# Optimization experiments

Measured on AMD Instinct MI355X. Metric: run time of the kernel, lower is better.

## Reference

```python
import jax, jax.numpy as jnp
import numpy as np

LN_EPS = 1e-12
BIG = 1e30
BAND = 15  # end index may be at most 15 tokens after start


def output_layer(x, w1, b1, g, b, w2, b2):
    # Linear -> ReLU -> LayerNorm -> Linear (dropout is identity at eval)
    h = jax.nn.relu(x @ w1 + b1)
    mu = jnp.mean(h, axis=-1, keepdims=True)
    var = jnp.mean(jnp.square(h - mu), axis=-1, keepdims=True)
    h = (h - mu) * jax.lax.rsqrt(var + LN_EPS) * g + b
    return h @ w2 + b2


def setup_inputs() -> dict:
    key = jax.random.key(0)
    ks = jax.random.split(key, 8)
    B, S, D = 8, 4096, 1024
    H2 = 2 * D
    inp = {
        "context_input": jax.random.normal(ks[0], (B, S, D), jnp.float32),
        "context_mask": jnp.ones((B, S), jnp.float32),
    }
    def head(k1, k2, n_ans):
        return (
            0.02 * jax.random.normal(k1, (D, H2), jnp.float32),
            jnp.zeros((H2,), jnp.float32),
            jnp.ones((H2,), jnp.float32),
            jnp.zeros((H2,), jnp.float32),
            0.02 * jax.random.normal(k2, (H2, n_ans), jnp.float32),
            jnp.zeros((n_ans,), jnp.float32),
        )
    for name, k1, k2, n_ans in [("start", ks[1], ks[2], 1), ("end", ks[3], ks[4], 1), ("type", ks[5], ks[6], 4)]:
        w1, b1, g, b, w2, b2 = head(k1, k2, n_ans)
        inp[f"{name}_w1"] = w1; inp[f"{name}_b1"] = b1
        inp[f"{name}_g"] = g; inp[f"{name}_b"] = b
        inp[f"{name}_w2"] = w2; inp[f"{name}_b2"] = b2
    return inp


def reference(context_input, context_mask,
              start_w1, start_b1, start_g, start_b, start_w2, start_b2,
              end_w1, end_b1, end_g, end_b, end_w2, end_b2,
              type_w1, type_b1, type_g, type_b, type_w2, type_b2):
    S = context_input.shape[1]
    start_pred = output_layer(context_input, start_w1, start_b1, start_g, start_b, start_w2, start_b2)[..., 0] \
        - BIG * (1.0 - context_mask)  # [B,S]
    end_pred = output_layer(context_input, end_w1, end_b1, end_g, end_b, end_w2, end_b2)[..., 0] \
        - BIG * (1.0 - context_mask)  # [B,S]
    type_pred = output_layer(context_input[:, 0, :], type_w1, type_b1, type_g, type_b, type_w2, type_b2)  # [B,4]

    # outer[b,i,j] = start[b,i] + end[b,j], masked to band 0 <= j-i <= 15
    outer = start_pred[:, :, None] + end_pred[:, None, :]  # [B,S,S]
    i = jnp.arange(S)[:, None]
    j = jnp.arange(S)[None, :]
    band = ((j >= i) & (j <= i + BAND)).astype(outer.dtype)  # [S,S]
    outer = outer - BIG * (1.0 - band)[None]

    yp1 = jnp.argmax(jnp.max(outer, axis=2), axis=1)  # best start index [B]
    yp2 = jnp.argmax(jnp.max(outer, axis=1), axis=1)  # best end index [B]
    return start_pred, end_pred, type_pred, yp1, yp2
```

## Files before the change

kernel.cpp:

```cpp
#include <hip/hip_runtime.h>

typedef _Float16 f16x8 __attribute__((ext_vector_type(8)));
typedef float f32x4 __attribute__((ext_vector_type(4)));

#define BIGF 1e30f
#define M_TOT 32768
#define H2 2048

#define WS_XH 0u
#define WS_WT 67108864u
#define WS_BVEC 75497472u
#define WS_GW2 75513856u
#define WS_CONSTS 75530240u
#define WS_PART 75530496u
#define WS_TPART 100696320u

__global__ void k_pre(const float* __restrict__ x, _Float16* __restrict__ xh,
                      const float* __restrict__ w_s, const float* __restrict__ w_e,
                      _Float16* __restrict__ wt,
                      const float* __restrict__ s_b1, const float* __restrict__ s_g,
                      const float* __restrict__ s_w2, const float* __restrict__ s_b,
                      const float* __restrict__ s_b2, const float* __restrict__ e_b1,
                      const float* __restrict__ e_g, const float* __restrict__ e_w2,
                      const float* __restrict__ e_b, const float* __restrict__ e_b2,
                      float* __restrict__ bvec, float* __restrict__ gw2,
                      float* __restrict__ consts) {
  __shared__ float tile[64][65];
  int bid = blockIdx.x;
  if (bid < 16384) {
    size_t i = ((size_t)bid * 256 + threadIdx.x) * 8;
    float4 v0 = *(const float4*)(x + i);
    float4 v1 = *(const float4*)(x + i + 4);
    f16x8 h;
    h[0] = (_Float16)v0.x; h[1] = (_Float16)v0.y; h[2] = (_Float16)v0.z; h[3] = (_Float16)v0.w;
    h[4] = (_Float16)v1.x; h[5] = (_Float16)v1.y; h[6] = (_Float16)v1.z; h[7] = (_Float16)v1.w;
    *(f16x8*)(xh + i) = h;
  } else if (bid < 17408) {
    int r = bid - 16384;
    int bx = r & 31, by = (r >> 5) & 15, bz = r >> 9;
    const float* w = bz ? w_e : w_s;
    int n0 = bx * 64, k0 = by * 64;
    int tx = threadIdx.x & 63, ty = threadIdx.x >> 6;
#pragma unroll
    for (int i = ty; i < 64; i += 4) tile[i][tx] = w[(size_t)(k0 + i) * H2 + n0 + tx];
    __syncthreads();
#pragma unroll
    for (int i = ty; i < 64; i += 4)
      wt[((size_t)(bz * H2 + n0 + i)) * 1024 + k0 + tx] = (_Float16)tile[tx][i];
  } else {
    int blk = bid - 17408;
    if (blk < 16) {
      int i = blk * 256 + threadIdx.x;
      int head = i >> 11, j = i & (H2 - 1);
      bvec[i] = head ? e_b1[j] : s_b1[j];
      gw2[i] = head ? e_g[j] * e_w2[j] : s_g[j] * s_w2[j];
    } else {
      int h = blk - 16;
      const float* g = h ? e_g : s_g;
      const float* b = h ? e_b : s_b;
      const float* w2 = h ? e_w2 : s_w2;
      const float* b2 = h ? e_b2 : s_b2;
      float c1 = 0.f, c2 = 0.f;
      for (int j = threadIdx.x; j < H2; j += 256) {
        float w = w2[j];
        c1 += g[j] * w;
        c2 += b[j] * w;
      }
      for (int m = 1; m < 64; m <<= 1) { c1 += __shfl_xor(c1, m); c2 += __shfl_xor(c2, m); }
      __shared__ float r1[4], r2[4];
      int wid = threadIdx.x >> 6;
      if ((threadIdx.x & 63) == 0) { r1[wid] = c1; r2[wid] = c2; }
      __syncthreads();
      if (threadIdx.x == 0) {
        consts[h * 2 + 0] = r1[0] + r1[1] + r1[2] + r1[3];
        consts[h * 2 + 1] = r2[0] + r2[1] + r2[2] + r2[3] + b2[0];
      }
    }
  }
}

#define BUF 65536
#define STA(q, tile, bufo)                                                              \
  __builtin_amdgcn_global_load_lds(                                                     \
      (const __attribute__((address_space(1))) unsigned int*)(srcA + (size_t)(q) * 131072 + (size_t)(tile) * 128), \
      (__attribute__((address_space(3))) unsigned int*)(lds + (bufo) + (q) * 8192 + t * 16), 16, 0, 0)
#define STB(q, tile, bufo)                                                              \
  __builtin_amdgcn_global_load_lds(                                                     \
      (const __attribute__((address_space(1))) unsigned int*)(srcB + (size_t)(q) * 131072 + (size_t)(tile) * 128), \
      (__attribute__((address_space(3))) unsigned int*)(lds + (bufo) + 32768 + (q) * 8192 + t * 16), 16, 0, 0)

#define READA(AF, mi0, BUFO)                                                            \
  AF[0][0] = *(const f16x8*)(lds + (BUFO) + arow + (mi0) * 2048 + low0);                \
  AF[0][1] = *(const f16x8*)(lds + (BUFO) + arow + (mi0) * 2048 + low1);                \
  AF[1][0] = *(const f16x8*)(lds + (BUFO) + arow + ((mi0) + 1) * 2048 + low0);          \
  AF[1][1] = *(const f16x8*)(lds + (BUFO) + arow + ((mi0) + 1) * 2048 + low1);

#define READB(BF, BUFO)                                                                 \
  _Pragma("unroll")                                                                     \
  for (int nj = 0; nj < 4; ++nj) {                                                      \
    BF[nj][0] = *(const f16x8*)(lds + (BUFO) + brow + nj * 2048 + low0);                \
    BF[nj][1] = *(const f16x8*)(lds + (BUFO) + brow + nj * 2048 + low1);                \
  }

#define MFMA2(m0, m1, AF, BF)                                                           \
  __builtin_amdgcn_s_setprio(1);                                                        \
  _Pragma("unroll")                                                                     \
  for (int nj = 0; nj < 4; ++nj) {                                                      \
    acc[m0][nj] = __builtin_amdgcn_mfma_f32_16x16x32_f16(AF[0][0], BF[nj][0], acc[m0][nj], 0, 0, 0); \
    acc[m1][nj] = __builtin_amdgcn_mfma_f32_16x16x32_f16(AF[1][0], BF[nj][0], acc[m1][nj], 0, 0, 0); \
  }                                                                                     \
  _Pragma("unroll")                                                                     \
  for (int nj = 0; nj < 4; ++nj) {                                                      \
    acc[m0][nj] = __builtin_amdgcn_mfma_f32_16x16x32_f16(AF[0][1], BF[nj][1], acc[m0][nj], 0, 0, 0); \
    acc[m1][nj] = __builtin_amdgcn_mfma_f32_16x16x32_f16(AF[1][1], BF[nj][1], acc[m1][nj], 0, 0, 0); \
  }                                                                                     \
  __builtin_amdgcn_s_setprio(0);

#define K_ITER(g, OB, OBN, BFC, BFN)                                                    \
  {                                                                                     \
                           \
    READA(afB, 2, OB);                                                                  \
    if ((g) < 15) { STA(1, (g) + 1, OBN); STA(3, (g) + 1, OBN); }                       \
    asm volatile("s_waitcnt lgkmcnt(4)" ::: "memory");                                  \
    __builtin_amdgcn_s_barrier();                                                       \
    __builtin_amdgcn_sched_barrier(0);                                                  \
    MFMA2(0, 1, afA, BFC);                                                              \
                           \
    READA(afA, 4, OB);                                                                  \
    if ((g) < 14) { STB(0, (g) + 2, OB); STB(1, (g) + 2, OB); }                         \
    asm volatile("s_waitcnt lgkmcnt(4)" ::: "memory");                                  \
    __builtin_amdgcn_s_barrier();                                                       \
    __builtin_amdgcn_sched_barrier(0);                                                  \
    MFMA2(2, 3, afB, BFC);                                                              \
           \
    READA(afB, 6, OB);                                                                  \
    if ((g) < 14) { STB(2, (g) + 2, OB); STB(3, (g) + 2, OB); }                         \
    if ((g) < 14)       asm volatile("s_waitcnt vmcnt(4)" ::: "memory");                \
    else if ((g) == 14) asm volatile("s_waitcnt vmcnt(0)" ::: "memory");                \
    asm volatile("s_waitcnt lgkmcnt(4)" ::: "memory");                                  \
    __builtin_amdgcn_s_barrier();                                                       \
    __builtin_amdgcn_sched_barrier(0);                                                  \
    MFMA2(4, 5, afA, BFC);                                                              \
       \
    if ((g) < 15) {                                                                     \
      READB(BFN, OBN);                                                                  \
      READA(afA, 0, OBN);                                                               \
      if ((g) < 14) { STA(0, (g) + 2, OB); STA(2, (g) + 2, OB); }                       \
      asm volatile("s_waitcnt lgkmcnt(12)" ::: "memory");                               \
    } else {                                                                            \
      asm volatile("s_waitcnt lgkmcnt(0)" ::: "memory");                                \
    }                                                                                   \
    __builtin_amdgcn_s_barrier();                                                       \
    __builtin_amdgcn_sched_barrier(0);                                                  \
    MFMA2(6, 7, afB, BFC);                                                              \
  }

__global__ __launch_bounds__(512, 2) void k_gemm(const _Float16* __restrict__ Xh,
                                                 const _Float16* __restrict__ Wt,
                                                 const float* __restrict__ bvec,
                                                 const float* __restrict__ gw2,
                                                 float* __restrict__ partials) {
  __shared__ char lds[2 * BUF];
  const int nb = blockIdx.x;
  const int mb = blockIdx.y;
  const int t = threadIdx.x;
  const int lane = t & 63, wid = t >> 6;
  const int c15 = lane & 15, g4 = lane >> 4;
  const int wmg = wid >> 2;
  const int wq = wid & 3;
  const int wn = wq * 64;

  f32x4 acc[8][4];
#pragma unroll
  for (int i = 0; i < 8; ++i)
#pragma unroll
    for (int j = 0; j < 4; ++j) acc[i][j] = (f32x4){0.f, 0.f, 0.f, 0.f};

  const char* Abase = (const char*)(Xh + (size_t)mb * 256 * 1024);
  const char* Bbase = (const char*)(Wt + (size_t)nb * 256 * 1024);
  const int rowl = t >> 3;
  const int swz = ((t & 7) * 16) ^ ((rowl & 7) << 4);
  const char* srcA = Abase + (size_t)rowl * 2048 + swz;
  const char* srcB = Bbase + (size_t)rowl * 2048 + swz;

  const int xorv = (c15 & 7) << 4;
  const int low0 = (g4 * 16) ^ xorv;
  const int low1 = (64 + g4 * 16) ^ xorv;
  const int arow = (wmg * 128 + c15) * 128;
  const int brow = 32768 + (wn + c15) * 128;

  STA(0, 0, 0); STA(1, 0, 0); STA(2, 0, 0); STA(3, 0, 0);
  STB(0, 0, 0); STB(1, 0, 0); STB(2, 0, 0); STB(3, 0, 0);
  STB(0, 1, BUF); STB(1, 1, BUF); STB(2, 1, BUF); STB(3, 1, BUF);
  STA(0, 1, BUF); STA(2, 1, BUF);
  asm volatile("s_waitcnt vmcnt(6)" ::: "memory");
  __builtin_amdgcn_s_barrier();
  __builtin_amdgcn_sched_barrier(0);

  f16x8 afA[2][2], afB[2][2], bfA[4][2], bfB[4][2];
  READB(bfA, 0);
  READA(afA, 0, 0);

#pragma unroll
  for (int gp = 0; gp < 8; ++gp) {
    K_ITER(2 * gp, 0u, BUF, bfA, bfB);
    K_ITER(2 * gp + 1, BUF, 0u, bfB, bfA);
  }

  __syncthreads();
  float* red = (float*)lds;

  float bv[4], gv[4];
#pragma unroll
  for (int nj = 0; nj < 4; ++nj) {
    int col = nb * 256 + wn + nj * 16 + c15;
    bv[nj] = bvec[col];
    gv[nj] = gw2[col];
  }
#pragma unroll
  for (int mi = 0; mi < 8; ++mi) {
#pragma unroll
    for (int r = 0; r < 4; ++r) {
      float s1 = 0.f, s2 = 0.f, s3 = 0.f;
#pragma unroll
      for (int nj = 0; nj < 4; ++nj) {
        float v = acc[mi][nj][r] + bv[nj];
        v = fmaxf(v, 0.f);
        s1 += v;
        s2 += v * v;
        s3 += v * gv[nj];
      }
#pragma unroll
      for (int m = 1; m < 16; m <<= 1) {
        s1 += __shfl_xor(s1, m);
        s2 += __shfl_xor(s2, m);
        s3 += __shfl_xor(s3, m);
      }
      if (c15 == 0) {
        int row = mi * 16 + g4 * 4 + r;
        float* p = red + (((wmg * 4 + wq) * 128 + row) * 3);
        p[0] = s1; p[1] = s2; p[2] = s3;
      }
    }
  }
  __syncthreads();
  for (int idx = t; idx < 768; idx += 512) {
    int wmgi = idx / 384;
    int rem = idx - wmgi * 384;
    int row = rem / 3, k = rem - row * 3;
    float s = red[((wmgi * 4 + 0) * 128 + row) * 3 + k] +
              red[((wmgi * 4 + 1) * 128 + row) * 3 + k] +
              red[((wmgi * 4 + 2) * 128 + row) * 3 + k] +
              red[((wmgi * 4 + 3) * 128 + row) * 3 + k];
    int rowg = mb * 256 + wmgi * 128 + row;
    partials[((size_t)(nb * 3 + k)) * M_TOT + rowg] = s;
  }
}

__global__ void k_reduce(const float* __restrict__ partials, const float* __restrict__ consts,
                         const float* __restrict__ mask, float* __restrict__ out) {
  int m = blockIdx.x * 256 + threadIdx.x;
  float s1 = 0.f, s2 = 0.f, s3 = 0.f, e1 = 0.f, e2 = 0.f, e3 = 0.f;
  for (int nb = 0; nb < 8; ++nb) {
    s1 += partials[((size_t)(nb * 3 + 0)) * M_TOT + m];
    s2 += partials[((size_t)(nb * 3 + 1)) * M_TOT + m];
    s3 += partials[((size_t)(nb * 3 + 2)) * M_TOT + m];
  }
  for (int nb = 8; nb < 16; ++nb) {
    e1 += partials[((size_t)(nb * 3 + 0)) * M_TOT + m];
    e2 += partials[((size_t)(nb * 3 + 1)) * M_TOT + m];
    e3 += partials[((size_t)(nb * 3 + 2)) * M_TOT + m];
  }
  const float H = (float)H2;
  float mu = s1 / H;
  float var = fmaxf(s2 / H - mu * mu, 0.f);
  float rs = 1.f / sqrtf(var + 1e-12f);
  float score_s = rs * (s3 - mu * consts[0]) + consts[1];
  mu = e1 / H;
  var = fmaxf(e2 / H - mu * mu, 0.f);
  rs = 1.f / sqrtf(var + 1e-12f);
  float score_e = rs * (e3 - mu * consts[2]) + consts[3];
  float mk = BIGF * (1.f - mask[m]);
  out[m] = score_s - mk;
  out[M_TOT + m] = score_e - mk;
}

__global__ void k_type_partial(const float* __restrict__ X, const float* __restrict__ w1,
                               const float* __restrict__ b1, const float* __restrict__ g,
                               const float* __restrict__ w2, float* __restrict__ tpart) {
  __shared__ float xs[1024];
  int cb = blockIdx.x, tok = blockIdx.y, t = threadIdx.x;
  const float* xp = X + (size_t)tok * 4096 * 1024;
  for (int i = t; i < 1024; i += 256) xs[i] = xp[i];
  __syncthreads();
  int j = cb * 256 + t;
  float dot = 0.f;
  for (int k = 0; k < 1024; ++k) dot += xs[k] * w1[(size_t)k * H2 + j];
  float h = fmaxf(dot + b1[j], 0.f);
  float gj = g[j];
  float s[6];
  s[0] = h;
  s[1] = h * h;
#pragma unroll
  for (int c = 0; c < 4; ++c) s[2 + c] = h * gj * w2[j * 4 + c];
  for (int m = 1; m < 64; m <<= 1)
#pragma unroll
    for (int q = 0; q < 6; ++q) s[q] += __shfl_xor(s[q], m);
  __shared__ float red[4][6];
  int wid = t >> 6;
  if ((t & 63) == 0)
#pragma unroll
    for (int q = 0; q < 6; ++q) red[wid][q] = s[q];
  __syncthreads();
  if (t == 0)
#pragma unroll
    for (int q = 0; q < 6; ++q)
      tpart[(tok * 8 + cb) * 6 + q] = red[0][q] + red[1][q] + red[2][q] + red[3][q];
}

__global__ void k_type_final(const float* __restrict__ tpart, const float* __restrict__ g,
                             const float* __restrict__ bb, const float* __restrict__ w2,
                             const float* __restrict__ b2, float* __restrict__ out) {
  int t = threadIdx.x;
  float c1[4] = {0.f, 0.f, 0.f, 0.f}, c2[4] = {0.f, 0.f, 0.f, 0.f};
  for (int j = t; j < H2; j += 256) {
    float gj = g[j], bj = bb[j];
#pragma unroll
    for (int c = 0; c < 4; ++c) {
      float w = w2[j * 4 + c];
      c1[c] += gj * w;
      c2[c] += bj * w;
    }
  }
  for (int m = 1; m < 64; m <<= 1)
#pragma unroll
    for (int c = 0; c < 4; ++c) { c1[c] += __shfl_xor(c1[c], m); c2[c] += __shfl_xor(c2[c], m); }
  __shared__ float rC1[4][4], rC2[4][4];
  int wid = t >> 6;
  if ((t & 63) == 0)
#pragma unroll
    for (int c = 0; c < 4; ++c) { rC1[wid][c] = c1[c]; rC2[wid][c] = c2[c]; }
  __syncthreads();
  __shared__ float sC1[4], sC2[4];
  if (t < 4) {
    sC1[t] = rC1[0][t] + rC1[1][t] + rC1[2][t] + rC1[3][t];
    sC2[t] = rC2[0][t] + rC2[1][t] + rC2[2][t] + rC2[3][t];
  }
  __syncthreads();
  if (t < 32) {
    int tok = t >> 2, c = t & 3;
    float s1 = 0.f, s2 = 0.f, s3 = 0.f;
    for (int cb = 0; cb < 8; ++cb) {
      s1 += tpart[(tok * 8 + cb) * 6 + 0];
      s2 += tpart[(tok * 8 + cb) * 6 + 1];
      s3 += tpart[(tok * 8 + cb) * 6 + 2 + c];
    }
    float mu = s1 / (float)H2;
    float var = fmaxf(s2 / (float)H2 - mu * mu, 0.f);
    float rs = 1.f / sqrtf(var + 1e-12f);
    out[65536 + tok * 4 + c] = rs * (s3 - mu * sC1[c]) + sC2[c] + b2[c];
  }
}

__global__ void k_band(const float* __restrict__ preds, float* __restrict__ out) {
  __shared__ float ss[4096], se[4096];
  int b = blockIdx.x, t = threadIdx.x;
  for (int i = t; i < 4096; i += 256) {
    ss[i] = preds[(size_t)b * 4096 + i];
    se[i] = preds[M_TOT + (size_t)b * 4096 + i];
  }
  __syncthreads();
  float bv1 = -3.0e38f, bv2 = -3.0e38f;
  int bi1 = 0x7fffffff, bi2 = 0x7fffffff;
  for (int i = t; i < 4096; i += 256) {
    float m1 = -3.0e38f;
    int jmax = i + 15 < 4095 ? i + 15 : 4095;
    for (int j = i; j <= jmax; ++j) m1 = fmaxf(m1, se[j]);
    float v1 = ss[i] + m1;
    if (v1 > bv1 || (v1 == bv1 && i < bi1)) { bv1 = v1; bi1 = i; }
    float m2 = -3.0e38f;
    int imin = i - 15 > 0 ? i - 15 : 0;
    for (int j = imin; j <= i; ++j) m2 = fmaxf(m2, ss[j]);
    float v2 = se[i] + m2;
    if (v2 > bv2 || (v2 == bv2 && i < bi2)) { bv2 = v2; bi2 = i; }
  }
  for (int m = 1; m < 64; m <<= 1) {
    float ov = __shfl_xor(bv1, m);
    int oi = __shfl_xor(bi1, m);
    if (ov > bv1 || (ov == bv1 && oi < bi1)) { bv1 = ov; bi1 = oi; }
    ov = __shfl_xor(bv2, m);
    oi = __shfl_xor(bi2, m);
    if (ov > bv2 || (ov == bv2 && oi < bi2)) { bv2 = ov; bi2 = oi; }
  }
  __shared__ float rv[2][4];
  __shared__ int ri[2][4];
  int wid = t >> 6;
  if ((t & 63) == 0) { rv[0][wid] = bv1; ri[0][wid] = bi1; rv[1][wid] = bv2; ri[1][wid] = bi2; }
  __syncthreads();
  if (t == 0) {
    float v = rv[0][0];
    int ix = ri[0][0];
    for (int w = 1; w < 4; ++w)
      if (rv[0][w] > v || (rv[0][w] == v && ri[0][w] < ix)) { v = rv[0][w]; ix = ri[0][w]; }
    out[65568 + b] = (float)ix;
    v = rv[1][0];
    ix = ri[1][0];
    for (int w = 1; w < 4; ++w)
      if (rv[1][w] > v || (rv[1][w] == v && ri[1][w] < ix)) { v = rv[1][w]; ix = ri[1][w]; }
    out[65576 + b] = (float)ix;
  }
}

extern "C" void kernel_launch(void* const* d_in, const int* in_sizes, int n_in, void* d_out,
                              int out_size, void* d_ws, size_t ws_size, hipStream_t stream) {
  const float* X = (const float*)d_in[0];
  const float* mask = (const float*)d_in[1];
  const float* s_w1 = (const float*)d_in[2];
  const float* s_b1 = (const float*)d_in[3];
  const float* s_g = (const float*)d_in[4];
  const float* s_b = (const float*)d_in[5];
  const float* s_w2 = (const float*)d_in[6];
  const float* s_b2 = (const float*)d_in[7];
  const float* e_w1 = (const float*)d_in[8];
  const float* e_b1 = (const float*)d_in[9];
  const float* e_g = (const float*)d_in[10];
  const float* e_b = (const float*)d_in[11];
  const float* e_w2 = (const float*)d_in[12];
  const float* e_b2 = (const float*)d_in[13];
  const float* t_w1 = (const float*)d_in[14];
  const float* t_b1 = (const float*)d_in[15];
  const float* t_g = (const float*)d_in[16];
  const float* t_b = (const float*)d_in[17];
  const float* t_w2 = (const float*)d_in[18];
  const float* t_b2 = (const float*)d_in[19];

  char* ws = (char*)d_ws;
  _Float16* Xh = (_Float16*)(ws + WS_XH);
  _Float16* Wt = (_Float16*)(ws + WS_WT);
  float* bvec = (float*)(ws + WS_BVEC);
  float* gw2 = (float*)(ws + WS_GW2);
  float* consts = (float*)(ws + WS_CONSTS);
  float* partials = (float*)(ws + WS_PART);
  float* tpart = (float*)(ws + WS_TPART);
  float* out = (float*)d_out;

  k_pre<<<17426, 256, 0, stream>>>(X, Xh, s_w1, e_w1, Wt, s_b1, s_g, s_w2, s_b, s_b2,
                                   e_b1, e_g, e_w2, e_b, e_b2, bvec, gw2, consts);
  k_gemm<<<dim3(16, 128), 512, 0, stream>>>(Xh, Wt, bvec, gw2, partials);
  k_reduce<<<128, 256, 0, stream>>>(partials, consts, mask, out);
  k_type_partial<<<dim3(8, 8), 256, 0, stream>>>(X, t_w1, t_b1, t_g, t_w2, tpart);
  k_type_final<<<1, 256, 0, stream>>>(tpart, t_g, t_b, t_w2, t_b2, out);
  k_band<<<8, 256, 0, stream>>>(out, out);
}
```

Measured before the change: 395.5 us.

## Restructure GEMM main loop into K-half phases with 4x4 MFMA blocks

Reorganizes the fp16 MFMA GEMM inner loop so each phase covers one K-half (low0/low1) across four M sub-tiles and four N sub-tiles. Each phase issues 16 MFMAs, where the previous code split the work by pairs of M rows across both K halves. Global-to-LDS prefetch of the next-next tile is regrouped behind a full vmcnt(0) wait and extra barriers around each MFMA block, and the loop runs with pragma unroll 2 instead of being fully unrolled. The aim is better LDS read reuse and fewer register fragments. The extra barriers and the full vmcnt wait may reduce overlap of loads with compute.

After: 869.5 us. +119.8%, slower.

```diff
diff --git a/kernel.cpp b/kernel.cpp
--- a/kernel.cpp
+++ b/kernel.cpp
@@ -89,71 +89,30 @@
       (const __attribute__((address_space(1))) unsigned int*)(srcB + (size_t)(q) * 131072 + (size_t)(tile) * 128), \
       (__attribute__((address_space(3))) unsigned int*)(lds + (bufo) + 32768 + (q) * 8192 + t * 16), 16, 0, 0)
 
-#define READA(AF, mi0, BUFO)                                                            \
-  AF[0][0] = *(const f16x8*)(lds + (BUFO) + arow + (mi0) * 2048 + low0);                \
-  AF[0][1] = *(const f16x8*)(lds + (BUFO) + arow + (mi0) * 2048 + low1);                \
-  AF[1][0] = *(const f16x8*)(lds + (BUFO) + arow + ((mi0) + 1) * 2048 + low0);          \
-  AF[1][1] = *(const f16x8*)(lds + (BUFO) + arow + ((mi0) + 1) * 2048 + low1);
-
-#define READB(BF, BUFO)                                                                 \
+#define RD_A(AF, mh, low, BUFO)                                                         \
   _Pragma("unroll")                                                                     \
-  for (int nj = 0; nj < 4; ++nj) {                                                      \
-    BF[nj][0] = *(const f16x8*)(lds + (BUFO) + brow + nj * 2048 + low0);                \
-    BF[nj][1] = *(const f16x8*)(lds + (BUFO) + brow + nj * 2048 + low1);                \
-  }
-
-#define MFMA2(m0, m1, AF, BF)                                                           \
+  for (int mi = 0; mi < 4; ++mi)                                                        \
+    AF[mi] = *(const f16x8*)(lds + (BUFO) + (unsigned)((wmg * 128 + (mh) * 64 + mi * 16 + c15) * 128) + (low));
+
+#define RD_B(BF, low, BUFO)                                                             \
+  _Pragma("unroll")                                                                     \
+  for (int nj = 0; nj < 4; ++nj)                                                        \
+    BF[nj] = *(const f16x8*)(lds + (BUFO) + 32768 + (unsigned)((wn + nj * 16 + c15) * 128) + (low));
+
+#define MF16(mh, AF, BF)                                                                \
   __builtin_amdgcn_s_setprio(1);                                                        \
   _Pragma("unroll")                                                                     \
-  for (int nj = 0; nj < 4; ++nj) {                                                      \
-    acc[m0][nj] = __builtin_amdgcn_mfma_f32_16x16x32_f16(AF[0][0], BF[nj][0], acc[m0][nj], 0, 0, 0); \
-    acc[m1][nj] = __builtin_amdgcn_mfma_f32_16x16x32_f16(AF[1][0], BF[nj][0], acc[m1][nj], 0, 0, 0); \
-  }                                                                                     \
-  _Pragma("unroll")                                                                     \
-  for (int nj = 0; nj < 4; ++nj) {                                                      \
-    acc[m0][nj] = __builtin_amdgcn_mfma_f32_16x16x32_f16(AF[0][1], BF[nj][1], acc[m0][nj], 0, 0, 0); \
-    acc[m1][nj] = __builtin_amdgcn_mfma_f32_16x16x32_f16(AF[1][1], BF[nj][1], acc[m1][nj], 0, 0, 0); \
-  }                                                                                     \
+  for (int mi = 0; mi < 4; ++mi)                                                        \
+    _Pragma("unroll")                                                                   \
+    for (int nj = 0; nj < 4; ++nj)                                                      \
+      acc[(mh) * 4 + mi][nj] =                                                          \
+          __builtin_amdgcn_mfma_f32_16x16x32_f16(AF[mi], BF[nj], acc[(mh) * 4 + mi][nj], 0, 0, 0); \
   __builtin_amdgcn_s_setprio(0);
 
-#define K_ITER(g, OB, OBN, BFC, BFN)                                                    \
-  {                                                                                     \
-                           \
-    READA(afB, 2, OB);                                                                  \
-    if ((g) < 15) { STA(1, (g) + 1, OBN); STA(3, (g) + 1, OBN); }                       \
-    asm volatile("s_waitcnt lgkmcnt(4)" ::: "memory");                                  \
-    __builtin_amdgcn_s_barrier();                                                       \
-    __builtin_amdgcn_sched_barrier(0);                                                  \
-    MFMA2(0, 1, afA, BFC);                                                              \
-                           \
-    READA(afA, 4, OB);                                                                  \
-    if ((g) < 14) { STB(0, (g) + 2, OB); STB(1, (g) + 2, OB); }                         \
-    asm volatile("s_waitcnt lgkmcnt(4)" ::: "memory");                                  \
-    __builtin_amdgcn_s_barrier();                                                       \
-    __builtin_amdgcn_sched_barrier(0);                                                  \
-    MFMA2(2, 3, afB, BFC);                                                              \
-           \
-    READA(afB, 6, OB);                                                                  \
-    if ((g) < 14) { STB(2, (g) + 2, OB); STB(3, (g) + 2, OB); }                         \
-    if ((g) < 14)       asm volatile("s_waitcnt vmcnt(4)" ::: "memory");                \
-    else if ((g) == 14) asm volatile("s_waitcnt vmcnt(0)" ::: "memory");                \
-    asm volatile("s_waitcnt lgkmcnt(4)" ::: "memory");                                  \
-    __builtin_amdgcn_s_barrier();                                                       \
-    __builtin_amdgcn_sched_barrier(0);                                                  \
-    MFMA2(4, 5, afA, BFC);                                                              \
-       \
-    if ((g) < 15) {                                                                     \
-      READB(BFN, OBN);                                                                  \
-      READA(afA, 0, OBN);                                                               \
-      if ((g) < 14) { STA(0, (g) + 2, OB); STA(2, (g) + 2, OB); }                       \
-      asm volatile("s_waitcnt lgkmcnt(12)" ::: "memory");                               \
-    } else {                                                                            \
-      asm volatile("s_waitcnt lgkmcnt(0)" ::: "memory");                                \
-    }                                                                                   \
-    __builtin_amdgcn_s_barrier();                                                       \
-    __builtin_amdgcn_sched_barrier(0);                                                  \
-    MFMA2(6, 7, afB, BFC);                                                              \
-  }
+#define LGKM_BAR(N)                                                                     \
+  asm volatile("s_waitcnt lgkmcnt(" #N ")" ::: "memory");                               \
+  __builtin_amdgcn_s_barrier();                                                         \
+  __builtin_amdgcn_sched_barrier(0);
 
 __global__ __launch_bounds__(512, 2) void k_gemm(const _Float16* __restrict__ Xh,
                                                  const _Float16* __restrict__ Wt,
@@ -184,27 +143,63 @@
   const char* srcB = Bbase + (size_t)rowl * 2048 + swz;
 
   const int xorv = (c15 & 7) << 4;
-  const int low0 = (g4 * 16) ^ xorv;
-  const int low1 = (64 + g4 * 16) ^ xorv;
-  const int arow = (wmg * 128 + c15) * 128;
-  const int brow = 32768 + (wn + c15) * 128;
+  const unsigned low0 = (unsigned)((g4 * 16) ^ xorv);
+  const unsigned low1 = (unsigned)((64 + g4 * 16) ^ xorv);
 
   STA(0, 0, 0); STA(1, 0, 0); STA(2, 0, 0); STA(3, 0, 0);
   STB(0, 0, 0); STB(1, 0, 0); STB(2, 0, 0); STB(3, 0, 0);
+  STA(0, 1, BUF); STA(1, 1, BUF); STA(2, 1, BUF); STA(3, 1, BUF);
   STB(0, 1, BUF); STB(1, 1, BUF); STB(2, 1, BUF); STB(3, 1, BUF);
-  STA(0, 1, BUF); STA(2, 1, BUF);
-  asm volatile("s_waitcnt vmcnt(6)" ::: "memory");
+  asm volatile("s_waitcnt vmcnt(8)" ::: "memory");
   __builtin_amdgcn_s_barrier();
   __builtin_amdgcn_sched_barrier(0);
 
-  f16x8 afA[2][2], afB[2][2], bfA[4][2], bfB[4][2];
-  READB(bfA, 0);
-  READA(afA, 0, 0);
-
-#pragma unroll
-  for (int gp = 0; gp < 8; ++gp) {
-    K_ITER(2 * gp, 0u, BUF, bfA, bfB);
-    K_ITER(2 * gp + 1, BUF, 0u, bfB, bfA);
+  f16x8 afA[4], afB[4], bfA[4], bfB[4];
+  RD_A(afA, 0, low0, 0u)
+  RD_B(bfA, low0, 0u)
+
+#pragma unroll 2
+  for (int g = 0; g < 16; ++g) {
+    const unsigned ob = (unsigned)(g & 1) * BUF;
+    const unsigned on = ob ^ BUF;
+
+    RD_A(afB, 1, low0, ob)
+    LGKM_BAR(4)
+    MF16(0, afA, bfA)
+    __builtin_amdgcn_s_barrier();
+    __builtin_amdgcn_sched_barrier(0);
+
+    RD_A(afA, 0, low1, ob)
+    RD_B(bfB, low1, ob)
+    LGKM_BAR(8)
+    MF16(1, afB, bfA)
+    __builtin_amdgcn_s_barrier();
+    __builtin_amdgcn_sched_barrier(0);
+
+    RD_A(afB, 1, low1, ob)
+    asm volatile("s_waitcnt lgkmcnt(4)" ::: "memory");
+    if (g < 15) asm volatile("s_waitcnt vmcnt(0)" ::: "memory");
+    __builtin_amdgcn_s_barrier();
+    __builtin_amdgcn_sched_barrier(0);
+    if (g < 14) {
+      STB(0, g + 2, ob); STB(1, g + 2, ob); STB(2, g + 2, ob); STB(3, g + 2, ob);
+      STA(0, g + 2, ob); STA(1, g + 2, ob);
+    }
+    MF16(0, afA, bfB)
+    __builtin_amdgcn_s_barrier();
+    __builtin_amdgcn_sched_barrier(0);
+
+    if (g < 15) {
+      RD_A(afA, 0, low0, on)
+      RD_B(bfA, low0, on)
+      LGKM_BAR(8)
+    } else {
+      LGKM_BAR(0)
+    }
+    if (g < 14) { STA(2, g + 2, ob); STA(3, g + 2, ob); }
+    MF16(1, afB, bfB)
+    __builtin_amdgcn_s_barrier();
+    __builtin_amdgcn_sched_barrier(0);
   }
 
   __syncthreads();
```

## Swizzle GEMM block order and merge small tail kernels into two launches

Applied to the files above, without the earlier changes.

The GEMM grid becomes 1D with a block-index swizzle, so consecutive blocks are spread across M-tiles in a pattern meant to improve L2 reuse of the weight and activation tiles (and possibly XCD placement). The reduce and type-head partial kernels are merged into one launch using block-index branching, and the type-final and band-argmax kernels are merged into a second. This cuts the launch count from five to three, removing launch gaps between tiny kernels, at the cost of larger shared-memory use per block in the fused kernels.

New measurement: 389.9 us, median of 3. Within noise of the previous version (-1.4%).

```diff
diff --git a/kernel.cpp b/kernel.cpp
--- a/kernel.cpp
+++ b/kernel.cpp
@@ -161,8 +161,10 @@
                                                  const float* __restrict__ gw2,
                                                  float* __restrict__ partials) {
   __shared__ char lds[2 * BUF];
-  const int nb = blockIdx.x;
-  const int mb = blockIdx.y;
+  const int bid = blockIdx.x;
+  const int swzb = (bid & 7) * 256 + (bid >> 3);
+  const int nb = swzb & 15;
+  const int mb = swzb >> 4;
   const int t = threadIdx.x;
   const int lane = t & 63, wid = t >> 6;
   const int c15 = lane & 15, g4 = lane >> 4;
@@ -257,157 +259,161 @@
   }
 }
 
-__global__ void k_reduce(const float* __restrict__ partials, const float* __restrict__ consts,
-                         const float* __restrict__ mask, float* __restrict__ out) {
-  int m = blockIdx.x * 256 + threadIdx.x;
-  float s1 = 0.f, s2 = 0.f, s3 = 0.f, e1 = 0.f, e2 = 0.f, e3 = 0.f;
-  for (int nb = 0; nb < 8; ++nb) {
-    s1 += partials[((size_t)(nb * 3 + 0)) * M_TOT + m];
-    s2 += partials[((size_t)(nb * 3 + 1)) * M_TOT + m];
-    s3 += partials[((size_t)(nb * 3 + 2)) * M_TOT + m];
-  }
-  for (int nb = 8; nb < 16; ++nb) {
-    e1 += partials[((size_t)(nb * 3 + 0)) * M_TOT + m];
-    e2 += partials[((size_t)(nb * 3 + 1)) * M_TOT + m];
-    e3 += partials[((size_t)(nb * 3 + 2)) * M_TOT + m];
-  }
-  const float H = (float)H2;
-  float mu = s1 / H;
-  float var = fmaxf(s2 / H - mu * mu, 0.f);
-  float rs = 1.f / sqrtf(var + 1e-12f);
-  float score_s = rs * (s3 - mu * consts[0]) + consts[1];
-  mu = e1 / H;
-  var = fmaxf(e2 / H - mu * mu, 0.f);
-  rs = 1.f / sqrtf(var + 1e-12f);
-  float score_e = rs * (e3 - mu * consts[2]) + consts[3];
-  float mk = BIGF * (1.f - mask[m]);
-  out[m] = score_s - mk;
-  out[M_TOT + m] = score_e - mk;
+__global__ void k_mid(const float* __restrict__ partials, const float* __restrict__ consts,
+                      const float* __restrict__ mask, float* __restrict__ out,
+                      const float* __restrict__ X, const float* __restrict__ w1,
+                      const float* __restrict__ b1, const float* __restrict__ g,
+                      const float* __restrict__ w2, float* __restrict__ tpart) {
+  __shared__ float xs[1024];
+  __shared__ float red[4][6];
+  int bid = blockIdx.x, t = threadIdx.x;
+  if (bid < 128) {
+    int m = bid * 256 + t;
+    float s1 = 0.f, s2 = 0.f, s3 = 0.f, e1 = 0.f, e2 = 0.f, e3 = 0.f;
+    for (int nb = 0; nb < 8; ++nb) {
+      s1 += partials[((size_t)(nb * 3 + 0)) * M_TOT + m];
+      s2 += partials[((size_t)(nb * 3 + 1)) * M_TOT + m];
+      s3 += partials[((size_t)(nb * 3 + 2)) * M_TOT + m];
+    }
+    for (int nb = 8; nb < 16; ++nb) {
+      e1 += partials[((size_t)(nb * 3 + 0)) * M_TOT + m];
+      e2 += partials[((size_t)(nb * 3 + 1)) * M_TOT + m];
+      e3 += partials[((size_t)(nb * 3 + 2)) * M_TOT + m];
+    }
+    const float H = (float)H2;
+    float mu = s1 / H;
+    float var = fmaxf(s2 / H - mu * mu, 0.f);
+    float rs = 1.f / sqrtf(var + 1e-12f);
+    float score_s = rs * (s3 - mu * consts[0]) + consts[1];
+    mu = e1 / H;
+    var = fmaxf(e2 / H - mu * mu, 0.f);
+    rs = 1.f / sqrtf(var + 1e-12f);
+    float score_e = rs * (e3 - mu * consts[2]) + consts[3];
+    float mk = BIGF * (1.f - mask[m]);
+    out[m] = score_s - mk;
+    out[M_TOT + m] = score_e - mk;
+  } else {
+    int r = bid - 128;
+    int cb = r & 7, tok = r >> 3;
+    const float* xp = X + (size_t)tok * 4096 * 1024;
+    for (int i = t; i < 1024; i += 256) xs[i] = xp[i];
+    __syncthreads();
+    int j = cb * 256 + t;
+    float dot = 0.f;
+    for (int k = 0; k < 1024; ++k) dot += xs[k] * w1[(size_t)k * H2 + j];
+    float h = fmaxf(dot + b1[j], 0.f);
+    float gj = g[j];
+    float s[6];
+    s[0] = h;
+    s[1] = h * h;
+#pragma unroll
+    for (int c = 0; c < 4; ++c) s[2 + c] = h * gj * w2[j * 4 + c];
+    for (int m = 1; m < 64; m <<= 1)
+#pragma unroll
+      for (int q = 0; q < 6; ++q) s[q] += __shfl_xor(s[q], m);
+    int wid = t >> 6;
+    if ((t & 63) == 0)
+#pragma unroll
+      for (int q = 0; q < 6; ++q) red[wid][q] = s[q];
+    __syncthreads();
+    if (t == 0)
+#pragma unroll
+      for (int q = 0; q < 6; ++q)
+        tpart[(tok * 8 + cb) * 6 + q] = red[0][q] + red[1][q] + red[2][q] + red[3][q];
+  }
 }
 
-__global__ void k_type_partial(const float* __restrict__ X, const float* __restrict__ w1,
-                               const float* __restrict__ b1, const float* __restrict__ g,
-                               const float* __restrict__ w2, float* __restrict__ tpart) {
-  __shared__ float xs[1024];
-  int cb = blockIdx.x, tok = blockIdx.y, t = threadIdx.x;
-  const float* xp = X + (size_t)tok * 4096 * 1024;
-  for (int i = t; i < 1024; i += 256) xs[i] = xp[i];
-  __syncthreads();
-  int j = cb * 256 + t;
-  float dot = 0.f;
-  for (int k = 0; k < 1024; ++k) dot += xs[k] * w1[(size_t)k * H2 + j];
-  float h = fmaxf(dot + b1[j], 0.f);
-  float gj = g[j];
-  float s[6];
-  s[0] = h;
-  s[1] = h * h;
-#pragma unroll
-  for (int c = 0; c < 4; ++c) s[2 + c] = h * gj * w2[j * 4 + c];
-  for (int m = 1; m < 64; m <<= 1)
-#pragma unroll
-    for (int q = 0; q < 6; ++q) s[q] += __shfl_xor(s[q], m);
-  __shared__ float red[4][6];
-  int wid = t >> 6;
-  if ((t & 63) == 0)
-#pragma unroll
-    for (int q = 0; q < 6; ++q) red[wid][q] = s[q];
-  __syncthreads();
-  if (t == 0)
-#pragma unroll
-    for (int q = 0; q < 6; ++q)
-      tpart[(tok * 8 + cb) * 6 + q] = red[0][q] + red[1][q] + red[2][q] + red[3][q];
-}
-
-__global__ void k_type_final(const float* __restrict__ tpart, const float* __restrict__ g,
-                             const float* __restrict__ bb, const float* __restrict__ w2,
-                             const float* __restrict__ b2, float* __restrict__ out) {
-  int t = threadIdx.x;
-  float c1[4] = {0.f, 0.f, 0.f, 0.f}, c2[4] = {0.f, 0.f, 0.f, 0.f};
-  for (int j = t; j < H2; j += 256) {
-    float gj = g[j], bj = bb[j];
-#pragma unroll
-    for (int c = 0; c < 4; ++c) {
-      float w = w2[j * 4 + c];
-      c1[c] += gj * w;
-      c2[c] += bj * w;
-    }
-  }
-  for (int m = 1; m < 64; m <<= 1)
-#pragma unroll
-    for (int c = 0; c < 4; ++c) { c1[c] += __shfl_xor(c1[c], m); c2[c] += __shfl_xor(c2[c], m); }
+__global__ void k_fin(const float* __restrict__ tpart, const float* __restrict__ g,
+                      const float* __restrict__ bb, const float* __restrict__ w2,
+                      const float* __restrict__ b2, float* __restrict__ out) {
+  __shared__ float ss[4096], se[4096];
   __shared__ float rC1[4][4], rC2[4][4];
-  int wid = t >> 6;
-  if ((t & 63) == 0)
-#pragma unroll
-    for (int c = 0; c < 4; ++c) { rC1[wid][c] = c1[c]; rC2[wid][c] = c2[c]; }
-  __syncthreads();
   __shared__ float sC1[4], sC2[4];
-  if (t < 4) {
-    sC1[t] = rC1[0][t] + rC1[1][t] + rC1[2][t] + rC1[3][t];
-    sC2[t] = rC2[0][t] + rC2[1][t] + rC2[2][t] + rC2[3][t];
-  }
-  __syncthreads();
-  if (t < 32) {
-    int tok = t >> 2, c = t & 3;
-    float s1 = 0.f, s2 = 0.f, s3 = 0.f;
-    for (int cb = 0; cb < 8; ++cb) {
-      s1 += tpart[(tok * 8 + cb) * 6 + 0];
-      s2 += tpart[(tok * 8 + cb) * 6 + 1];
-      s3 += tpart[(tok * 8 + cb) * 6 + 2 + c];
-    }
-    float mu = s1 / (float)H2;
-    float var = fmaxf(s2 / (float)H2 - mu * mu, 0.f);
-    float rs = 1.f / sqrtf(var + 1e-12f);
-    out[65536 + tok * 4 + c] = rs * (s3 - mu * sC1[c]) + sC2[c] + b2[c];
-  }
-}
-
-__global__ void k_band(const float* __restrict__ preds, float* __restrict__ out) {
-  __shared__ float ss[4096], se[4096];
-  int b = blockIdx.x, t = threadIdx.x;
-  for (int i = t; i < 4096; i += 256) {
-    ss[i] = preds[(size_t)b * 4096 + i];
-    se[i] = preds[M_TOT + (size_t)b * 4096 + i];
-  }
-  __syncthreads();
-  float bv1 = -3.0e38f, bv2 = -3.0e38f;
-  int bi1 = 0x7fffffff, bi2 = 0x7fffffff;
-  for (int i = t; i < 4096; i += 256) {
-    float m1 = -3.0e38f;
-    int jmax = i + 15 < 4095 ? i + 15 : 4095;
-    for (int j = i; j <= jmax; ++j) m1 = fmaxf(m1, se[j]);
-    float v1 = ss[i] + m1;
-    if (v1 > bv1 || (v1 == bv1 && i < bi1)) { bv1 = v1; bi1 = i; }
-    float m2 = -3.0e38f;
-    int imin = i - 15 > 0 ? i - 15 : 0;
-    for (int j = imin; j <= i; ++j) m2 = fmaxf(m2, ss[j]);
-    float v2 = se[i] + m2;
-    if (v2 > bv2 || (v2 == bv2 && i < bi2)) { bv2 = v2; bi2 = i; }
-  }
-  for (int m = 1; m < 64; m <<= 1) {
-    float ov = __shfl_xor(bv1, m);
-    int oi = __shfl_xor(bi1, m);
-    if (ov > bv1 || (ov == bv1 && oi < bi1)) { bv1 = ov; bi1 = oi; }
-    ov = __shfl_xor(bv2, m);
-    oi = __shfl_xor(bi2, m);
-    if (ov > bv2 || (ov == bv2 && oi < bi2)) { bv2 = ov; bi2 = oi; }
-  }
   __shared__ float rv[2][4];
   __shared__ int ri[2][4];
-  int wid = t >> 6;
-  if ((t & 63) == 0) { rv[0][wid] = bv1; ri[0][wid] = bi1; rv[1][wid] = bv2; ri[1][wid] = bi2; }
-  __syncthreads();
-  if (t == 0) {
-    float v = rv[0][0];
-    int ix = ri[0][0];
-    for (int w = 1; w < 4; ++w)
-      if (rv[0][w] > v || (rv[0][w] == v && ri[0][w] < ix)) { v = rv[0][w]; ix = ri[0][w]; }
-    out[65568 + b] = (float)ix;
-    v = rv[1][0];
-    ix = ri[1][0];
-    for (int w = 1; w < 4; ++w)
-      if (rv[1][w] > v || (rv[1][w] == v && ri[1][w] < ix)) { v = rv[1][w]; ix = ri[1][w]; }
-    out[65576 + b] = (float)ix;
+  int bid = blockIdx.x, t = threadIdx.x;
+  if (bid == 0) {
+    float c1[4] = {0.f, 0.f, 0.f, 0.f}, c2[4] = {0.f, 0.f, 0.f, 0.f};
+    for (int j = t; j < H2; j += 256) {
+      float gj = g[j], bj = bb[j];
+#pragma unroll
+      for (int c = 0; c < 4; ++c) {
+        float w = w2[j * 4 + c];
+        c1[c] += gj * w;
+        c2[c] += bj * w;
+      }
+    }
+    for (int m = 1; m < 64; m <<= 1)
+#pragma unroll
+      for (int c = 0; c < 4; ++c) { c1[c] += __shfl_xor(c1[c], m); c2[c] += __shfl_xor(c2[c], m); }
+    int wid = t >> 6;
+    if ((t & 63) == 0)
+#pragma unroll
+      for (int c = 0; c < 4; ++c) { rC1[wid][c] = c1[c]; rC2[wid][c] = c2[c]; }
+    __syncthreads();
+    if (t < 4) {
+      sC1[t] = rC1[0][t] + rC1[1][t] + rC1[2][t] + rC1[3][t];
+      sC2[t] = rC2[0][t] + rC2[1][t] + rC2[2][t] + rC2[3][t];
+    }
+    __syncthreads();
+    if (t < 32) {
+      int tok = t >> 2, c = t & 3;
+      float s1 = 0.f, s2 = 0.f, s3 = 0.f;
+      for (int cb = 0; cb < 8; ++cb) {
+        s1 += tpart[(tok * 8 + cb) * 6 + 0];
+        s2 += tpart[(tok * 8 + cb) * 6 + 1];
+        s3 += tpart[(tok * 8 + cb) * 6 + 2 + c];
+      }
+      float mu = s1 / (float)H2;
+      float var = fmaxf(s2 / (float)H2 - mu * mu, 0.f);
+      float rs = 1.f / sqrtf(var + 1e-12f);
+      out[65536 + tok * 4 + c] = rs * (s3 - mu * sC1[c]) + sC2[c] + b2[c];
+    }
+  } else {
+    int b = bid - 1;
+    const float* preds = out;
+    for (int i = t; i < 4096; i += 256) {
+      ss[i] = preds[(size_t)b * 4096 + i];
+      se[i] = preds[M_TOT + (size_t)b * 4096 + i];
+    }
+    __syncthreads();
+    float bv1 = -3.0e38f, bv2 = -3.0e38f;
+    int bi1 = 0x7fffffff, bi2 = 0x7fffffff;
+    for (int i = t; i < 4096; i += 256) {
+      float m1 = -3.0e38f;
+      int jmax = i + 15 < 4095 ? i + 15 : 4095;
+      for (int j = i; j <= jmax; ++j) m1 = fmaxf(m1, se[j]);
+      float v1 = ss[i] + m1;
+      if (v1 > bv1 || (v1 == bv1 && i < bi1)) { bv1 = v1; bi1 = i; }
+      float m2 = -3.0e38f;
+      int imin = i - 15 > 0 ? i - 15 : 0;
+      for (int j = imin; j <= i; ++j) m2 = fmaxf(m2, ss[j]);
+      float v2 = se[i] + m2;
+      if (v2 > bv2 || (v2 == bv2 && i < bi2)) { bv2 = v2; bi2 = i; }
+    }
+    for (int m = 1; m < 64; m <<= 1) {
+      float ov = __shfl_xor(bv1, m);
+      int oi = __shfl_xor(bi1, m);
+      if (ov > bv1 || (ov == bv1 && oi < bi1)) { bv1 = ov; bi1 = oi; }
+      ov = __shfl_xor(bv2, m);
+      oi = __shfl_xor(bi2, m);
+      if (ov > bv2 || (ov == bv2 && oi < bi2)) { bv2 = ov; bi2 = oi; }
+    }
+    int wid = t >> 6;
+    if ((t & 63) == 0) { rv[0][wid] = bv1; ri[0][wid] = bi1; rv[1][wid] = bv2; ri[1][wid] = bi2; }
+    __syncthreads();
+    if (t == 0) {
+      float v = rv[0][0];
+      int ix = ri[0][0];
+      for (int w = 1; w < 4; ++w)
+        if (rv[0][w] > v || (rv[0][w] == v && ri[0][w] < ix)) { v = rv[0][w]; ix = ri[0][w]; }
+      out[65568 + b] = (float)ix;
+      v = rv[1][0];
+      ix = ri[1][0];
+      for (int w = 1; w < 4; ++w)
+        if (rv[1][w] > v || (rv[1][w] == v && ri[1][w] < ix)) { v = rv[1][w]; ix = ri[1][w]; }
+      out[65576 + b] = (float)ix;
+    }
   }
 }
 
@@ -446,9 +452,7 @@
 
   k_pre<<<17426, 256, 0, stream>>>(X, Xh, s_w1, e_w1, Wt, s_b1, s_g, s_w2, s_b, s_b2,
                                    e_b1, e_g, e_w2, e_b, e_b2, bvec, gw2, consts);
-  k_gemm<<<dim3(16, 128), 512, 0, stream>>>(Xh, Wt, bvec, gw2, partials);
-  k_reduce<<<128, 256, 0, stream>>>(partials, consts, mask, out);
-  k_type_partial<<<dim3(8, 8), 256, 0, stream>>>(X, t_w1, t_b1, t_g, t_w2, tpart);
-  k_type_final<<<1, 256, 0, stream>>>(tpart, t_g, t_b, t_w2, t_b2, out);
-  k_band<<<8, 256, 0, stream>>>(out, out);
+  k_gemm<<<2048, 512, 0, stream>>>(Xh, Wt, bvec, gw2, partials);
+  k_mid<<<192, 256, 0, stream>>>(partials, consts, mask, out, X, t_w1, t_b1, t_g, t_w2, tpart);
+  k_fin<<<9, 256, 0, stream>>>(tpart, t_g, t_b, t_w2, t_b2, out);
 }
```
